# Kernel tuning notes

Measured on AMD Instinct MI355X. Metric: run time of the kernel, lower is better.

## Reference

```python
import jax, jax.numpy as jnp
import numpy as np

N = 4096
IN_CH = 256
OUT_CH = 256
NUM_REL = 8


def setup_inputs() -> dict:
    key = jax.random.key(0)
    k_x, k_a, k_e, k_w = jax.random.split(key, 4)
    x = jax.random.normal(k_x, (N, IN_CH), dtype=jnp.float32)
    A = jax.random.uniform(k_a, (N, N), dtype=jnp.float32)
    edge_type = jax.random.randint(k_e, (N, N), 0, NUM_REL, dtype=jnp.int32)
    # xavier_uniform per-relation weight [R, in, out]
    limit = np.sqrt(6.0 / (IN_CH + OUT_CH))
    weight = jax.random.uniform(k_w, (NUM_REL, IN_CH, OUT_CH), dtype=jnp.float32,
                                minval=-limit, maxval=limit)
    bias = jnp.zeros((OUT_CH,), dtype=jnp.float32)
    return {"x": x, "A": A, "edge_type": edge_type, "weight": weight, "bias": bias}


def reference(x, A, edge_type, weight, bias):
    # out = sum_r ((A * [edge_type == r]) @ x) @ W_r + bias
    num_rel = weight.shape[0]
    out = jnp.zeros((x.shape[0], weight.shape[2]), dtype=x.dtype)
    for rel in range(num_rel):  # small fixed relation count
        rel_adj = A * (edge_type == rel).astype(x.dtype)   # [N, N]
        h = rel_adj @ x                                     # [N, in]
        out = out + h @ weight[rel]                         # [N, out]
    out = out + bias
    return out
```

## Files before the change

### kernel.cpp

```cpp
#include <hip/hip_runtime.h>
#include <stdint.h>


#define NN 4096

typedef __attribute__((ext_vector_type(8))) short  s16x8;
typedef __attribute__((ext_vector_type(4))) float  fx4;
typedef __attribute__((ext_vector_type(4))) unsigned int ux4;

union uq { ux4 u; s16x8 s; };

__device__ __forceinline__ unsigned short f2bf(float f) {
  union { float f; unsigned int u; } v; v.f = f;
  unsigned int r = v.u + 0x7fffu + ((v.u >> 16) & 1u);
  return (unsigned short)(r >> 16);
}

__device__ __forceinline__ void gld16(const void* g, void* l) {
  __builtin_amdgcn_global_load_lds(
      (const __attribute__((address_space(1))) unsigned int*)(uintptr_t)g,
      (__attribute__((address_space(3))) unsigned int*)(uintptr_t)l, 16, 0, 0);
}

__global__ void k_init(const float* __restrict__ bias, float* __restrict__ out) {
  int idx = blockIdx.x * 256 + threadIdx.x;
  out[idx] = bias[idx & 255];
}

__global__ __launch_bounds__(256, 2) void k_y(const float* __restrict__ x,
                                              const float* __restrict__ W,
                                              unsigned short* __restrict__ yt) {
  __shared__ unsigned short Wl[128 * 256];
  const int t  = threadIdx.x;
  const int j0 = blockIdx.x * 128;
  const int o0 = blockIdx.y * 16;

  {
    const int r = t >> 5, kc = t & 31;
#pragma unroll
    for (int u = 0; u < 8; ++u) {
      const int k = kc * 8 + u;
      const fx4* wp = (const fx4*)(W + ((size_t)r * 256 + k) * 256 + o0);
      fx4 w[4] = { wp[0], wp[1], wp[2], wp[3] };
#pragma unroll
      for (int i = 0; i < 16; ++i) {
        const int row = i * 8 + r;
        const int gs  = (k >> 3) ^ (row & 7);
        Wl[row * 256 + gs * 8 + (k & 7)] = f2bf(w[i >> 2][i & 3]);
      }
    }
  }
  __syncthreads();

  const int lane = t & 63, wid = t >> 6;
  const int l15 = lane & 15, lh = lane >> 4;
  const int npb = wid * 32;

  fx4 acc[8][2];
#pragma unroll
  for (int m = 0; m < 8; ++m)
#pragma unroll
    for (int n = 0; n < 2; ++n) acc[m][n] = 0.f;

  unsigned int qb[2];
#pragma unroll
  for (int n = 0; n < 2; ++n) {
    int row = npb + n * 16 + l15;
    qb[n] = (unsigned)(row * 512 + 16 * (lh ^ (row & 3))) ^ (64u * ((row >> 2) & 1));
  }
  const char* WlB = (const char*)Wl;
  const float* xb = x + (size_t)(j0 + l15) * 256 + lh * 8;

#pragma unroll
  for (int ks = 0; ks < 8; ++ks) {
    s16x8 a[8];
#pragma unroll
    for (int m = 0; m < 8; ++m) {
      const fx4* xp = (const fx4*)(xb + (size_t)m * 16 * 256 + ks * 32);
      fx4 x0 = xp[0], x1 = xp[1];
      s16x8 av;
#pragma unroll
      for (int i = 0; i < 4; ++i) av[i] = (short)f2bf(x0[i]);
#pragma unroll
      for (int i = 0; i < 4; ++i) av[4 + i] = (short)f2bf(x1[i]);
      a[m] = av;
    }
#pragma unroll
    for (int n = 0; n < 2; ++n) {
      s16x8 b = *(const s16x8*)(WlB + (qb[n] ^ (unsigned)(ks * 64)));
#pragma unroll
      for (int m = 0; m < 8; ++m)
        acc[m][n] = __builtin_amdgcn_mfma_f32_16x16x32_bf16(a[m], b, acc[m][n], 0, 0, 0);
    }
  }

#pragma unroll
  for (int m = 0; m < 8; ++m)
#pragma unroll
    for (int n = 0; n < 2; ++n)
#pragma unroll
      for (int q = 0; q < 4; ++q) {
        int jl = m * 16 + lh * 4 + q;
        int np = npb + n * 16 + l15;
        int o  = o0 + (np >> 3);
        yt[(size_t)o * 32768 + (size_t)(j0 + jl) * 8 + (np & 7)] = f2bf(acc[m][n][q]);
      }
}

__global__ __launch_bounds__(256, 2) void k_main(const float* __restrict__ A,
                                                 const int*   __restrict__ et,
                                                 const unsigned short* __restrict__ yt,
                                                 float* __restrict__ out) {
  __shared__ ux4 smem[4608];
  const int t = threadIdx.x, lane = t & 63, w = t >> 6;
  const int l15 = lane & 15, lh = lane >> 4;
  const int wm = w >> 1, wn = w & 1;
  const int i0 = blockIdx.x * 128;
  const int o0 = blockIdx.y * 128;
  const int jb = blockIdx.z * 512;

  float* Af = (float*)smem;
  int*   Ef = (int*)((char*)smem + 12288);
  char*  Bc = (char*)smem + 24576;
  char*  smc = (char*)smem;

  const float* sA = A  + (size_t)(i0 + (t >> 1)) * NN + jb + (t & 1) * 4;
  const int*   sE = et + (size_t)(i0 + (t >> 1)) * NN + jb + (t & 1) * 4;
  const ux4* ytg = (const ux4*)yt;
  const ux4* sB[4];
#pragma unroll
  for (int u = 0; u < 4; ++u) {
    int row = w * 32 + u * 8 + (lane >> 3);
    int sl  = (lane & 7) ^ (row & 7);
    sB[u] = ytg + ((size_t)(o0 + row) << 12) + jb + sl;
  }

#define STAGE(sq, p) do {                                                 \
    gld16(sA + (size_t)(sq) * 8, smc + (p) * 4096 + w * 1024);            \
    gld16(sE + (size_t)(sq) * 8, smc + 12288 + (p) * 4096 + w * 1024);    \
    _Pragma("unroll")                                                     \
    for (int u = 0; u < 4; ++u)                                           \
      gld16(sB[u] + (size_t)(sq) * 8,                                     \
            Bc + (p) * 16384 + (w * 32 + u * 8) * 128);                   \
  } while (0)

  int ibase[4];
#pragma unroll
  for (int m = 0; m < 4; ++m)
    ibase[m] = (wm * 64 + m * 16 + l15) * 8 + lh;
  unsigned Qb[4];
#pragma unroll
  for (int n = 0; n < 4; ++n) {
    int row = wn * 64 + n * 16 + l15;
    Qb[n] = (unsigned)(row * 128 + ((lh ^ (row & 7)) << 4));
  }

  fx4 acc[4][4];
#pragma unroll
  for (int m = 0; m < 4; ++m)
#pragma unroll
    for (int n = 0; n < 4; ++n) acc[m][n] = 0.f;

  STAGE(0, 0);
  STAGE(1, 1);

  int p = 0;
  for (int s = 0; s < 64; ++s) {
    asm volatile("s_waitcnt vmcnt(6)" ::: "memory");
    __builtin_amdgcn_s_barrier();
    {
      int sq = (s + 2 > 63) ? 63 : s + 2;
      int p2 = p + 2; if (p2 >= 3) p2 -= 3;
      STAGE(sq, p2);
    }
    const int pW = p * 1024;
    const unsigned pB = (unsigned)(p * 16384);
    float aLo[4], aHi[4]; int eLo[4], eHi[4];
#pragma unroll
    for (int m = 0; m < 4; ++m) {
      int idx = pW + ibase[m];
      aLo[m] = Af[idx]; aHi[m] = Af[idx + 4];
      eLo[m] = Ef[idx]; eHi[m] = Ef[idx + 4];
    }
#pragma unroll
    for (int ks = 0; ks < 2; ++ks) {
      uq a4[4];
#pragma unroll
      for (int m = 0; m < 4; ++m) {
        float av = ks ? aHi[m] : aLo[m];
        int   ev = ks ? eHi[m] : eLo[m];
        unsigned long long sh = ((unsigned long long)f2bf(av)) << ((ev & 3) * 16);
        unsigned lo = (unsigned)sh, hi = (unsigned)(sh >> 32);
        bool c = ev < 4;
        ux4 q;
        q.x = c ? lo : 0u; q.y = c ? hi : 0u; q.z = c ? 0u : lo; q.w = c ? 0u : hi;
        a4[m].u = q;
      }
#pragma unroll
      for (int n = 0; n < 4; ++n) {
        uq b; b.u = *(const ux4*)(Bc + pB + (Qb[n] ^ (unsigned)(ks * 64)));
#pragma unroll
        for (int m = 0; m < 4; ++m)
          acc[m][n] = __builtin_amdgcn_mfma_f32_16x16x32_bf16(a4[m].s, b.s, acc[m][n], 0, 0, 0);
      }
    }
    p = (p == 2) ? 0 : p + 1;
  }
  asm volatile("s_waitcnt vmcnt(0)" ::: "memory");

#pragma unroll
  for (int m = 0; m < 4; ++m)
#pragma unroll
    for (int n = 0; n < 4; ++n)
#pragma unroll
      for (int q = 0; q < 4; ++q) {
        int gi = i0 + wm * 64 + m * 16 + lh * 4 + q;
        int go = o0 + wn * 64 + n * 16 + l15;
        atomicAdd(out + (size_t)gi * 256 + go, acc[m][n][q]);
      }
#undef STAGE
}

extern "C" void kernel_launch(void* const* d_in, const int* in_sizes, int n_in,
                              void* d_out, int out_size, void* d_ws, size_t ws_size,
                              hipStream_t stream) {
  const float* x    = (const float*)d_in[0];
  const float* A    = (const float*)d_in[1];
  const int*   et   = (const int*)d_in[2];
  const float* W    = (const float*)d_in[3];
  const float* bias = (const float*)d_in[4];
  float* out = (float*)d_out;
  unsigned short* yt = (unsigned short*)d_ws;

  k_init<<<dim3(4096), dim3(256), 0, stream>>>(bias, out);
  k_y   <<<dim3(32, 16), dim3(256), 0, stream>>>(x, W, yt);
  k_main<<<dim3(32, 2, 8), dim3(256), 0, stream>>>(A, et, yt, out);
}
```

Baseline: 144.5 us.

## Load A/edge_type directly to registers and switch main kernel to 32x32 MFMA

```diff
diff --git a/kernel.cpp b/kernel.cpp
--- a/kernel.cpp
+++ b/kernel.cpp
@@ -4,9 +4,11 @@
 
 #define NN 4096
 
-typedef __attribute__((ext_vector_type(8))) short  s16x8;
-typedef __attribute__((ext_vector_type(4))) float  fx4;
-typedef __attribute__((ext_vector_type(4))) unsigned int ux4;
+typedef __attribute__((ext_vector_type(8)))  short s16x8;
+typedef __attribute__((ext_vector_type(16))) float f32x16;
+typedef __attribute__((ext_vector_type(4)))  float fx4;
+typedef __attribute__((ext_vector_type(4)))  int   ix4;
+typedef __attribute__((ext_vector_type(4)))  unsigned int ux4;
 
 union uq { ux4 u; s16x8 s; };
 
@@ -111,114 +113,125 @@
                                                  const int*   __restrict__ et,
                                                  const unsigned short* __restrict__ yt,
                                                  float* __restrict__ out) {
-  __shared__ ux4 smem[4608];
+  __shared__ ux4 Bl[3 * 1024];
   const int t = threadIdx.x, lane = t & 63, w = t >> 6;
-  const int l15 = lane & 15, lh = lane >> 4;
+  const int l31 = lane & 31, lh1 = lane >> 5;
   const int wm = w >> 1, wn = w & 1;
   const int i0 = blockIdx.x * 128;
   const int o0 = blockIdx.y * 128;
   const int jb = blockIdx.z * 512;
 
-  float* Af = (float*)smem;
-  int*   Ef = (int*)((char*)smem + 12288);
-  char*  Bc = (char*)smem + 24576;
-  char*  smc = (char*)smem;
-
-  const float* sA = A  + (size_t)(i0 + (t >> 1)) * NN + jb + (t & 1) * 4;
-  const int*   sE = et + (size_t)(i0 + (t >> 1)) * NN + jb + (t & 1) * 4;
+  const fx4* pA[2]; const ix4* pE[2];
+#pragma unroll
+  for (int m = 0; m < 2; ++m) {
+    size_t off = (size_t)(i0 + wm * 64 + m * 32 + l31) * NN + jb + lh1 * 4;
+    pA[m] = (const fx4*)(A + off);
+    pE[m] = (const ix4*)(et + off);
+  }
+
   const ux4* ytg = (const ux4*)yt;
   const ux4* sB[4];
 #pragma unroll
   for (int u = 0; u < 4; ++u) {
     int row = w * 32 + u * 8 + (lane >> 3);
-    int sl  = (lane & 7) ^ (row & 7);
+    int sl  = (lane & 7) ^ ((lane >> 3) & 7);
     sB[u] = ytg + ((size_t)(o0 + row) << 12) + jb + sl;
   }
-
-#define STAGE(sq, p) do {                                                 \
-    gld16(sA + (size_t)(sq) * 8, smc + (p) * 4096 + w * 1024);            \
-    gld16(sE + (size_t)(sq) * 8, smc + 12288 + (p) * 4096 + w * 1024);    \
-    _Pragma("unroll")                                                     \
-    for (int u = 0; u < 4; ++u)                                           \
-      gld16(sB[u] + (size_t)(sq) * 8,                                     \
-            Bc + (p) * 16384 + (w * 32 + u * 8) * 128);                   \
+  char* Bc = (char*)Bl;
+
+  unsigned Qb[2];
+#pragma unroll
+  for (int n = 0; n < 2; ++n) {
+    int row = wn * 64 + n * 32 + l31;
+    Qb[n] = (unsigned)(row * 128 + (((lh1 * 4) ^ (row & 7)) << 4));
+  }
+
+  f32x16 acc[2][2];
+#pragma unroll
+  for (int m = 0; m < 2; ++m)
+#pragma unroll
+    for (int n = 0; n < 2; ++n) acc[m][n] = 0.f;
+
+#define ISSUE(sq, p, aset, eset) do {                                   \
+    _Pragma("unroll")                                                   \
+    for (int u = 0; u < 4; ++u)                                         \
+      gld16(sB[u] + (size_t)(sq) * 8,                                   \
+            Bc + (p) * 16384 + (w * 32 + u * 8) * 128);                 \
+    aset[0] = pA[0][(sq) * 2]; aset[1] = pA[1][(sq) * 2];               \
+    eset[0] = pE[0][(sq) * 2]; eset[1] = pE[1][(sq) * 2];               \
   } while (0)
 
-  int ibase[4];
-#pragma unroll
-  for (int m = 0; m < 4; ++m)
-    ibase[m] = (wm * 64 + m * 16 + l15) * 8 + lh;
-  unsigned Qb[4];
-#pragma unroll
-  for (int n = 0; n < 4; ++n) {
-    int row = wn * 64 + n * 16 + l15;
-    Qb[n] = (unsigned)(row * 128 + ((lh ^ (row & 7)) << 4));
-  }
-
-  fx4 acc[4][4];
-#pragma unroll
-  for (int m = 0; m < 4; ++m)
-#pragma unroll
-    for (int n = 0; n < 4; ++n) acc[m][n] = 0.f;
-
-  STAGE(0, 0);
-  STAGE(1, 1);
+#define BUILD(aset, eset, frag) do {                                    \
+    _Pragma("unroll")                                                   \
+    for (int m = 0; m < 2; ++m)                                         \
+      _Pragma("unroll")                                                 \
+      for (int ks = 0; ks < 4; ++ks) {                                  \
+        unsigned hv = f2bf(aset[m][ks]);                                \
+        int ev = eset[m][ks];                                           \
+        unsigned long long sh = ((unsigned long long)hv) << ((ev & 3) * 16); \
+        unsigned lo = (unsigned)sh, hi = (unsigned)(sh >> 32);          \
+        bool c = ev < 4;                                                \
+        ux4 q;                                                          \
+        q.x = c ? lo : 0u; q.y = c ? hi : 0u;                           \
+        q.z = c ? 0u : lo; q.w = c ? 0u : hi;                           \
+        frag[m][ks].u = q;                                              \
+      }                                                                 \
+  } while (0)
+
+#define COMPUTE(p, frag) do {                                           \
+    const unsigned pB = (unsigned)((p) * 16384);                        \
+    _Pragma("unroll")                                                   \
+    for (int ks = 0; ks < 4; ++ks) {                                    \
+      uq b0, b1;                                                        \
+      b0.u = *(const ux4*)(Bc + pB + (Qb[0] ^ (unsigned)(ks << 4)));    \
+      b1.u = *(const ux4*)(Bc + pB + (Qb[1] ^ (unsigned)(ks << 4)));    \
+      _Pragma("unroll")                                                 \
+      for (int m = 0; m < 2; ++m) {                                     \
+        acc[m][0] = __builtin_amdgcn_mfma_f32_32x32x16_bf16(frag[m][ks].s, b0.s, acc[m][0], 0, 0, 0); \
+        acc[m][1] = __builtin_amdgcn_mfma_f32_32x32x16_bf16(frag[m][ks].s, b1.s, acc[m][1], 0, 0, 0); \
+      }                                                                 \
+    }                                                                   \
+  } while (0)
+
+  fx4 aE[2], aO[2]; ix4 eE[2], eO[2];
+  uq fragE[2][4], fragO[2][4];
+
+  ISSUE(0, 0, aE, eE);
+  ISSUE(1, 1, aO, eO);
 
   int p = 0;
-  for (int s = 0; s < 64; ++s) {
-    asm volatile("s_waitcnt vmcnt(6)" ::: "memory");
+  for (int s = 0; s < 64; s += 2) {
+    int p1 = p + 1; if (p1 == 3) p1 = 0;
+    int p2 = p + 2; if (p2 >= 3) p2 -= 3;
+    int sq2 = (s + 2 > 63) ? 63 : s + 2;
+    int sq3 = (s + 3 > 63) ? 63 : s + 3;
+    asm volatile("s_waitcnt vmcnt(8)" ::: "memory");
     __builtin_amdgcn_s_barrier();
-    {
-      int sq = (s + 2 > 63) ? 63 : s + 2;
-      int p2 = p + 2; if (p2 >= 3) p2 -= 3;
-      STAGE(sq, p2);
-    }
-    const int pW = p * 1024;
-    const unsigned pB = (unsigned)(p * 16384);
-    float aLo[4], aHi[4]; int eLo[4], eHi[4];
-#pragma unroll
-    for (int m = 0; m < 4; ++m) {
-      int idx = pW + ibase[m];
-      aLo[m] = Af[idx]; aHi[m] = Af[idx + 4];
-      eLo[m] = Ef[idx]; eHi[m] = Ef[idx + 4];
-    }
-#pragma unroll
-    for (int ks = 0; ks < 2; ++ks) {
-      uq a4[4];
-#pragma unroll
-      for (int m = 0; m < 4; ++m) {
-        float av = ks ? aHi[m] : aLo[m];
-        int   ev = ks ? eHi[m] : eLo[m];
-        unsigned long long sh = ((unsigned long long)f2bf(av)) << ((ev & 3) * 16);
-        unsigned lo = (unsigned)sh, hi = (unsigned)(sh >> 32);
-        bool c = ev < 4;
-        ux4 q;
-        q.x = c ? lo : 0u; q.y = c ? hi : 0u; q.z = c ? 0u : lo; q.w = c ? 0u : hi;
-        a4[m].u = q;
-      }
-#pragma unroll
-      for (int n = 0; n < 4; ++n) {
-        uq b; b.u = *(const ux4*)(Bc + pB + (Qb[n] ^ (unsigned)(ks * 64)));
-#pragma unroll
-        for (int m = 0; m < 4; ++m)
-          acc[m][n] = __builtin_amdgcn_mfma_f32_16x16x32_bf16(a4[m].s, b.s, acc[m][n], 0, 0, 0);
-      }
-    }
-    p = (p == 2) ? 0 : p + 1;
+    BUILD(aE, eE, fragE);
+    ISSUE(sq2, p2, aE, eE);
+    COMPUTE(p, fragE);
+    asm volatile("s_waitcnt vmcnt(8)" ::: "memory");
+    __builtin_amdgcn_s_barrier();
+    BUILD(aO, eO, fragO);
+    ISSUE(sq3, p, aO, eO);
+    COMPUTE(p1, fragO);
+    p = p2;
   }
   asm volatile("s_waitcnt vmcnt(0)" ::: "memory");
 
 #pragma unroll
-  for (int m = 0; m < 4; ++m)
-#pragma unroll
-    for (int n = 0; n < 4; ++n)
-#pragma unroll
-      for (int q = 0; q < 4; ++q) {
-        int gi = i0 + wm * 64 + m * 16 + lh * 4 + q;
-        int go = o0 + wn * 64 + n * 16 + l15;
+  for (int m = 0; m < 2; ++m)
+#pragma unroll
+    for (int n = 0; n < 2; ++n)
+#pragma unroll
+      for (int q = 0; q < 16; ++q) {
+        int gi = i0 + wm * 64 + m * 32 + (q & 3) + 8 * (q >> 2) + 4 * lh1;
+        int go = o0 + wn * 64 + n * 32 + l31;
         atomicAdd(out + (size_t)gi * 256 + go, acc[m][n][q]);
       }
-#undef STAGE
+#undef ISSUE
+#undef BUILD
+#undef COMPUTE
 }
 
 extern "C" void kernel_launch(void* const* d_in, const int* in_sizes, int n_in,
```

After: 159.7 us. +10.5%, slower.

## Restructure main kernel into 256x256 tiles with 32x32 MFMA and register-staged A encoding

Applied to the files above, without the earlier changes.

```diff
diff --git a/kernel.cpp b/kernel.cpp
--- a/kernel.cpp
+++ b/kernel.cpp
@@ -4,9 +4,11 @@
 
 #define NN 4096
 
-typedef __attribute__((ext_vector_type(8))) short  s16x8;
-typedef __attribute__((ext_vector_type(4))) float  fx4;
-typedef __attribute__((ext_vector_type(4))) unsigned int ux4;
+typedef __attribute__((ext_vector_type(8)))  short s16x8;
+typedef __attribute__((ext_vector_type(16))) float f32x16;
+typedef __attribute__((ext_vector_type(4)))  float fx4;
+typedef __attribute__((ext_vector_type(4)))  int   ix4;
+typedef __attribute__((ext_vector_type(4)))  unsigned int ux4;
 
 union uq { ux4 u; s16x8 s; };
 
@@ -107,118 +109,116 @@
       }
 }
 
-__global__ __launch_bounds__(256, 2) void k_main(const float* __restrict__ A,
+__global__ __launch_bounds__(512, 2) void k_main(const float* __restrict__ A,
                                                  const int*   __restrict__ et,
                                                  const unsigned short* __restrict__ yt,
                                                  float* __restrict__ out) {
-  __shared__ ux4 smem[4608];
+  __shared__ ux4 smem[8192];
+  char* smc = (char*)smem;
   const int t = threadIdx.x, lane = t & 63, w = t >> 6;
-  const int l15 = lane & 15, lh = lane >> 4;
-  const int wm = w >> 1, wn = w & 1;
-  const int i0 = blockIdx.x * 128;
-  const int o0 = blockIdx.y * 128;
-  const int jb = blockIdx.z * 512;
-
-  float* Af = (float*)smem;
-  int*   Ef = (int*)((char*)smem + 12288);
-  char*  Bc = (char*)smem + 24576;
-  char*  smc = (char*)smem;
-
-  const float* sA = A  + (size_t)(i0 + (t >> 1)) * NN + jb + (t & 1) * 4;
-  const int*   sE = et + (size_t)(i0 + (t >> 1)) * NN + jb + (t & 1) * 4;
+  const int l31 = lane & 31, lh1 = lane >> 5;
+  const int wm = w >> 2, wn = w & 3;
+  const int i0 = blockIdx.x * 256;
+  const int jb = blockIdx.y * 256;
+
+  const int bi = t >> 1, bq = t & 1;
+  const fx4* pA = (const fx4*)(A  + (size_t)(i0 + bi) * NN + jb + bq * 4);
+  const ix4* pE = (const ix4*)(et + (size_t)(i0 + bi) * NN + jb + bq * 4);
+  unsigned awr[4];
+#pragma unroll
+  for (int k = 0; k < 4; ++k)
+    awr[k] = (unsigned)(bi * 128 + (((bq * 4 + k) ^ (bi & 7)) << 4));
+
   const ux4* ytg = (const ux4*)yt;
   const ux4* sB[4];
 #pragma unroll
   for (int u = 0; u < 4; ++u) {
-    int row = w * 32 + u * 8 + (lane >> 3);
-    int sl  = (lane & 7) ^ (row & 7);
-    sB[u] = ytg + ((size_t)(o0 + row) << 12) + jb + sl;
-  }
-
-#define STAGE(sq, p) do {                                                 \
-    gld16(sA + (size_t)(sq) * 8, smc + (p) * 4096 + w * 1024);            \
-    gld16(sE + (size_t)(sq) * 8, smc + 12288 + (p) * 4096 + w * 1024);    \
-    _Pragma("unroll")                                                     \
-    for (int u = 0; u < 4; ++u)                                           \
-      gld16(sB[u] + (size_t)(sq) * 8,                                     \
-            Bc + (p) * 16384 + (w * 32 + u * 8) * 128);                   \
-  } while (0)
-
-  int ibase[4];
+    int o  = w * 32 + u * 8 + (lane >> 3);
+    int sp = lane & 7;
+    sB[u] = ytg + ((size_t)o << 12) + jb + (sp ^ (o & 7));
+  }
+
+  unsigned QA[4], QB[2];
+#pragma unroll
+  for (int m = 0; m < 4; ++m) {
+    int ir = wm * 128 + m * 32 + l31;
+    QA[m] = (unsigned)(ir * 128 + ((lh1 ^ (ir & 7)) << 4));
+  }
+#pragma unroll
+  for (int n = 0; n < 2; ++n) {
+    int orow = wn * 64 + n * 32 + l31;
+    QB[n] = (unsigned)(65536 + orow * 128 + ((lh1 ^ (orow & 7)) << 4));
+  }
+
+  f32x16 acc[4][2];
 #pragma unroll
   for (int m = 0; m < 4; ++m)
-    ibase[m] = (wm * 64 + m * 16 + l15) * 8 + lh;
-  unsigned Qb[4];
-#pragma unroll
-  for (int n = 0; n < 4; ++n) {
-    int row = wn * 64 + n * 16 + l15;
-    Qb[n] = (unsigned)(row * 128 + ((lh ^ (row & 7)) << 4));
-  }
-
-  fx4 acc[4][4];
+#pragma unroll
+    for (int n = 0; n < 2; ++n) acc[m][n] = 0.f;
+
+  fx4 a0 = pA[0]; ix4 e0 = pE[0];
+#pragma unroll
+  for (int u = 0; u < 4; ++u)
+    gld16(sB[u], smc + 65536 + (w * 32 + u * 8) * 128);
+  fx4 aN = pA[2]; ix4 eN = pE[2];
+#pragma unroll
+  for (int k = 0; k < 4; ++k) {
+    unsigned long long sh = ((unsigned long long)f2bf(a0[k])) << ((e0[k] & 3) * 16);
+    unsigned lo = (unsigned)sh, hi = (unsigned)(sh >> 32);
+    bool c = e0[k] < 4;
+    ux4 q; q.x = c ? lo : 0u; q.y = c ? hi : 0u; q.z = c ? 0u : lo; q.w = c ? 0u : hi;
+    *(ux4*)(smc + awr[k]) = q;
+  }
+
+  for (int s = 0; s < 32; ++s) {
+    asm volatile("s_waitcnt vmcnt(2) lgkmcnt(0)" ::: "memory");
+    __builtin_amdgcn_s_barrier();
+    const int s1 = (s + 1 < 32) ? s + 1 : 31;
+    const int s2 = (s + 2 < 32) ? s + 2 : 31;
+    const unsigned bB = 65536u + (unsigned)(((s + 1) & 1) * 32768);
+#pragma unroll
+    for (int u = 0; u < 4; ++u)
+      gld16(sB[u] + (size_t)s1 * 8, smc + bB + (w * 32 + u * 8) * 128);
+    fx4 a2 = pA[2 * s2]; ix4 e2 = pE[2 * s2];
+    const unsigned bA = (unsigned)(((s + 1) & 1) * 32768);
+#pragma unroll
+    for (int k = 0; k < 4; ++k) {
+      unsigned long long sh = ((unsigned long long)f2bf(aN[k])) << ((eN[k] & 3) * 16);
+      unsigned lo = (unsigned)sh, hi = (unsigned)(sh >> 32);
+      bool c = eN[k] < 4;
+      ux4 q; q.x = c ? lo : 0u; q.y = c ? hi : 0u; q.z = c ? 0u : lo; q.w = c ? 0u : hi;
+      *(ux4*)(smc + bA + awr[k]) = q;
+    }
+    const unsigned cO = (unsigned)((s & 1) * 32768);
+#pragma unroll
+    for (int ks = 0; ks < 4; ++ks) {
+      uq a[4], b[2];
+#pragma unroll
+      for (int m = 0; m < 4; ++m)
+        a[m].u = *(const ux4*)(smc + cO + (QA[m] ^ (unsigned)(ks << 5)));
+#pragma unroll
+      for (int n = 0; n < 2; ++n)
+        b[n].u = *(const ux4*)(smc + cO + (QB[n] ^ (unsigned)(ks << 5)));
+#pragma unroll
+      for (int m = 0; m < 4; ++m)
+#pragma unroll
+        for (int n = 0; n < 2; ++n)
+          acc[m][n] = __builtin_amdgcn_mfma_f32_32x32x16_bf16(a[m].s, b[n].s, acc[m][n], 0, 0, 0);
+    }
+    aN = a2; eN = e2;
+  }
+  asm volatile("s_waitcnt vmcnt(0)" ::: "memory");
+
 #pragma unroll
   for (int m = 0; m < 4; ++m)
 #pragma unroll
-    for (int n = 0; n < 4; ++n) acc[m][n] = 0.f;
-
-  STAGE(0, 0);
-  STAGE(1, 1);
-
-  int p = 0;
-  for (int s = 0; s < 64; ++s) {
-    asm volatile("s_waitcnt vmcnt(6)" ::: "memory");
-    __builtin_amdgcn_s_barrier();
-    {
-      int sq = (s + 2 > 63) ? 63 : s + 2;
-      int p2 = p + 2; if (p2 >= 3) p2 -= 3;
-      STAGE(sq, p2);
-    }
-    const int pW = p * 1024;
-    const unsigned pB = (unsigned)(p * 16384);
-    float aLo[4], aHi[4]; int eLo[4], eHi[4];
-#pragma unroll
-    for (int m = 0; m < 4; ++m) {
-      int idx = pW + ibase[m];
-      aLo[m] = Af[idx]; aHi[m] = Af[idx + 4];
-      eLo[m] = Ef[idx]; eHi[m] = Ef[idx + 4];
-    }
-#pragma unroll
-    for (int ks = 0; ks < 2; ++ks) {
-      uq a4[4];
-#pragma unroll
-      for (int m = 0; m < 4; ++m) {
-        float av = ks ? aHi[m] : aLo[m];
-        int   ev = ks ? eHi[m] : eLo[m];
-        unsigned long long sh = ((unsigned long long)f2bf(av)) << ((ev & 3) * 16);
-        unsigned lo = (unsigned)sh, hi = (unsigned)(sh >> 32);
-        bool c = ev < 4;
-        ux4 q;
-        q.x = c ? lo : 0u; q.y = c ? hi : 0u; q.z = c ? 0u : lo; q.w = c ? 0u : hi;
-        a4[m].u = q;
-      }
-#pragma unroll
-      for (int n = 0; n < 4; ++n) {
-        uq b; b.u = *(const ux4*)(Bc + pB + (Qb[n] ^ (unsigned)(ks * 64)));
-#pragma unroll
-        for (int m = 0; m < 4; ++m)
-          acc[m][n] = __builtin_amdgcn_mfma_f32_16x16x32_bf16(a4[m].s, b.s, acc[m][n], 0, 0, 0);
-      }
-    }
-    p = (p == 2) ? 0 : p + 1;
-  }
-  asm volatile("s_waitcnt vmcnt(0)" ::: "memory");
-
-#pragma unroll
-  for (int m = 0; m < 4; ++m)
-#pragma unroll
-    for (int n = 0; n < 4; ++n)
-#pragma unroll
-      for (int q = 0; q < 4; ++q) {
-        int gi = i0 + wm * 64 + m * 16 + lh * 4 + q;
-        int go = o0 + wn * 64 + n * 16 + l15;
+    for (int n = 0; n < 2; ++n)
+#pragma unroll
+      for (int q = 0; q < 16; ++q) {
+        int gi = i0 + wm * 128 + m * 32 + (q & 3) + 8 * (q >> 2) + 4 * lh1;
+        int go = wn * 64 + n * 32 + l31;
         atomicAdd(out + (size_t)gi * 256 + go, acc[m][n][q]);
       }
-#undef STAGE
 }
 
 extern "C" void kernel_launch(void* const* d_in, const int* in_sizes, int n_in,
@@ -234,5 +234,5 @@
 
   k_init<<<dim3(4096), dim3(256), 0, stream>>>(bias, out);
   k_y   <<<dim3(32, 16), dim3(256), 0, stream>>>(x, W, yt);
-  k_main<<<dim3(32, 2, 8), dim3(256), 0, stream>>>(A, et, yt, out);
-}
+  k_main<<<dim3(16, 16), dim3(512), 0, stream>>>(A, et, yt, out);
+}
```

New measurement: 167.7 us. 16.0% more time.
